# Optimization experiments

Measured on AMD Instinct MI355X. Metric: run time of the kernel, lower is better.

## Reference

```python
import jax, jax.numpy as jnp
import numpy as np

G, N, E, F, H, O, MO = 64, 2048, 16384, 128, 128, 128, 128


def setup_inputs() -> dict:
    key = jax.random.key(0)
    ks = jax.random.split(key, 12)
    # edges: per-graph contiguous blocks, local indices in [0, N-2] (never touch center N-1)
    src_l = jax.random.randint(ks[0], (G, E), 0, N - 1)
    dst_l = jax.random.randint(ks[1], (G, E), 0, N - 1)
    offs = (jnp.arange(G, dtype=jnp.int64) * N)[:, None]
    edge_index = jnp.stack([(src_l + offs).reshape(-1), (dst_l + offs).reshape(-1)]).astype(jnp.int64)
    x = jax.random.normal(ks[2], (G * N, F), dtype=jnp.float32)
    batch = jnp.repeat(jnp.arange(G, dtype=jnp.int64), N)
    center_node_indices = jnp.full((G,), N - 1, dtype=jnp.int64)
    def lin(k, fan_in, shape):
        return jax.random.normal(k, shape, dtype=jnp.float32) / np.sqrt(fan_in)
    return {
        "x": x, "edge_index": edge_index, "batch": batch,
        "center_node_indices": center_node_indices,
        "W1": lin(ks[3], F, (F, H)), "b1": jnp.zeros((H,), jnp.float32),
        "W2": lin(ks[4], F, (F, O)), "b2": jnp.zeros((O,), jnp.float32),
        "W3": lin(ks[5], F, (F, O)), "b3": jnp.zeros((O,), jnp.float32),
        "Wm": lin(ks[6], H + F, (H + F, MO)), "bm": jnp.zeros((MO,), jnp.float32),
    }


def _gcn(x, src, dst, W, b):
    # PyG GCNConv: D^{-1/2}(A+I)D^{-1/2} X W + b, messages src->dst, deg at dst
    n = x.shape[0]
    h = x @ W
    deg = 1.0 + jax.ops.segment_sum(jnp.ones(src.shape[0], h.dtype), dst, num_segments=n)
    dis = jax.lax.rsqrt(deg)
    msg = h[src] * (dis[src] * dis[dst])[:, None]
    agg = jax.ops.segment_sum(msg, dst, num_segments=n)
    return agg + h * (1.0 / deg)[:, None] + b


_gcn_v = jax.vmap(_gcn, in_axes=(0, 0, 0, None, None))


def reference(x, edge_index, batch, center_node_indices, W1, b1, W2, b2, W3, b3, Wm, bm):
    g = center_node_indices.shape[0]
    n = x.shape[0] // g
    e = edge_index.shape[1] // g
    offs = (jnp.arange(g) * n)[:, None]
    src = edge_index[0].reshape(g, e) - offs  # local per-graph edges
    dst = edge_index[1].reshape(g, e) - offs
    xg = x.reshape(g, n, -1)                      # [G,N,F]
    h1 = _gcn_v(xg, src, dst, W1, b1)             # [G,N,H]
    ce = h1[jnp.arange(g), center_node_indices]   # [G,H] center embeddings
    x_nc = xg[:, : n - 1]                         # non-center nodes (center = N-1)
    hd = W1.shape[1]
    # MLP(cat([center_emb, node_feat])) = relu(ce@Wm_top + x@Wm_bot + bm)
    mask = jax.nn.relu((ce @ Wm[:hd])[:, None, :] + x_nc @ Wm[hd:] + bm)  # [G,N-1,MO]
    core = _gcn_v(mask * x_nc, src, dst, W2, b2)          # [G,N-1,O]
    red = _gcn_v((1.0 - mask) * x_nc, src, dst, W3, b3)   # [G,N-1,O]
    return core.mean(axis=0), red.mean(axis=0)
```

## Files before the change

kernel.cpp:

```cpp
#include <hip/hip_runtime.h>

typedef unsigned short u16;
typedef unsigned int uint32;
typedef __bf16 bf16x8 __attribute__((ext_vector_type(8)));
typedef float f32x4 __attribute__((ext_vector_type(4)));

static constexpr int Gg = 64;
static constexpr int Nn = 2048;
static constexpr int Ee = 16384;
static constexpr int GN = Gg * Nn;
static constexpr int GE = Gg * Ee;

__device__ __forceinline__ u16 f2u(float f) {
    uint32 i = __float_as_uint(f);
    uint32 r = (i + 0x7FFFu + ((i >> 16) & 1u)) >> 16;
    return (u16)r;
}
__device__ __forceinline__ float lo16f(uint32 v) { return __uint_as_float(v << 16); }
__device__ __forceinline__ float hi16f(uint32 v) { return __uint_as_float(v & 0xffff0000u); }

__global__ __launch_bounds__(1024) void k_build(const int* __restrict__ ei,
                                                const float* __restrict__ Wm,
                                                const float* __restrict__ x,
                                                const int* __restrict__ center,
                                                const float* __restrict__ W1,
                                                const float* __restrict__ b1,
                                                const float* __restrict__ bm,
                                                float* __restrict__ invdeg,
                                                int* __restrict__ rp, int2* __restrict__ nme,
                                                u16* __restrict__ Wtp,
                                                float* __restrict__ A) {
    int t = threadIdx.x;
    if (blockIdx.x >= 64) {
        int g = blockIdx.x - 64;
        __shared__ float sv[128], sce[128], spart[8][128];
        int seg = t >> 7, ch = t & 127;
        if (t < 128) {
            int cg = (g << 11) + center[g];
            sv[t] = x[cg * 128 + t];
        }
        __syncthreads();
        float p = 0.f;
        #pragma unroll
        for (int f0 = 0; f0 < 16; ++f0) {
            int f = seg * 16 + f0;
            p += sv[f] * W1[f * 128 + ch];
        }
        spart[seg][ch] = p;
        __syncthreads();
        if (t < 128) {
            float a = b1[t];
            #pragma unroll
            for (int s2 = 0; s2 < 8; ++s2) a += spart[s2][t];
            sce[t] = a;
        }
        __syncthreads();
        p = 0.f;
        #pragma unroll
        for (int f0 = 0; f0 < 16; ++f0) {
            int f = seg * 16 + f0;
            p += sce[f] * Wm[f * 128 + ch];
        }
        spart[seg][ch] = p;
        __syncthreads();
        if (t < 128) {
            float a = bm[t];
            #pragma unroll
            for (int s2 = 0; s2 < 8; ++s2) a += spart[s2][t];
            A[g * 128 + t] = a;
        }
        return;
    }

    int g = blockIdx.x;
    __shared__ int h[2048];
    __shared__ float sdis[2048];
    __shared__ int wsum[16];
    int* curs = h;
    h[t] = 0; h[t + 1024] = 0;
    if (t < 256) {
        int tid = g * 256 + t;
        int j = tid & 7, l = (tid >> 3) & 63, kc = tid >> 9;
        int ks = kc >> 3, ct = kc & 7, lm = l & 15, lq = l >> 4;
        int f = ks * 32 + lq * 8 + j, c = ct * 16 + lm;
        Wtp[tid] = f2u(Wm[(128 + f) * 128 + c]);
    }
    __syncthreads();
    #pragma unroll
    for (int k = 0; k < 4; ++k) {
        int4 d4 = *(const int4*)&ei[GE + g * Ee + k * 4096 + t * 4];
        atomicAdd(&h[d4.x & (Nn - 1)], 1);
        atomicAdd(&h[d4.y & (Nn - 1)], 1);
        atomicAdd(&h[d4.z & (Nn - 1)], 1);
        atomicAdd(&h[d4.w & (Nn - 1)], 1);
    }
    __syncthreads();
    int c0 = h[2 * t], c1 = h[2 * t + 1];
    {
        float d0 = 1.0f + (float)c0, d1 = 1.0f + (float)c1;
        sdis[2 * t] = rsqrtf(d0);
        sdis[2 * t + 1] = rsqrtf(d1);
        invdeg[(g << 11) + 2 * t] = 1.0f / d0;
        invdeg[(g << 11) + 2 * t + 1] = 1.0f / d1;
    }
    int val = c0 + c1;
    int lane = t & 63, wv = t >> 6;
    int inc = val;
    #pragma unroll
    for (int off = 1; off < 64; off <<= 1) {
        int n = __shfl_up(inc, off, 64);
        if (lane >= off) inc += n;
    }
    if (lane == 63) wsum[wv] = inc;
    __syncthreads();
    if (wv == 0 && lane < 16) {
        int s2 = wsum[lane];
        #pragma unroll
        for (int off = 1; off < 16; off <<= 1) {
            int n = __shfl_up(s2, off, 16);
            if ((lane & 15) >= off) s2 += n;
        }
        wsum[lane] = s2;
    }
    __syncthreads();
    int excl = inc - val + (wv ? wsum[wv - 1] : 0);
    int base = g * Ee + excl;
    rp[(g << 11) + 2 * t] = base;
    rp[(g << 11) + 2 * t + 1] = base + c0;
    if (g == 63 && t == 1023) rp[GN] = GE;
    curs[2 * t] = base;
    curs[2 * t + 1] = base + c0;
    __syncthreads();
    #pragma unroll
    for (int k = 0; k < 4; ++k) {
        int e = g * Ee + k * 4096 + t * 4;
        int4 s4 = *(const int4*)&ei[e];
        int4 d4 = *(const int4*)&ei[GE + e];
        int p0 = atomicAdd(&curs[d4.x & (Nn - 1)], 1);
        nme[p0] = make_int2(s4.x, __float_as_int(sdis[s4.x & (Nn - 1)] * sdis[d4.x & (Nn - 1)]));
        int p1 = atomicAdd(&curs[d4.y & (Nn - 1)], 1);
        nme[p1] = make_int2(s4.y, __float_as_int(sdis[s4.y & (Nn - 1)] * sdis[d4.y & (Nn - 1)]));
        int p2 = atomicAdd(&curs[d4.z & (Nn - 1)], 1);
        nme[p2] = make_int2(s4.z, __float_as_int(sdis[s4.z & (Nn - 1)] * sdis[d4.z & (Nn - 1)]));
        int p3 = atomicAdd(&curs[d4.w & (Nn - 1)], 1);
        nme[p3] = make_int2(s4.w, __float_as_int(sdis[s4.w & (Nn - 1)] * sdis[d4.w & (Nn - 1)]));
    }
}

__global__ __launch_bounds__(512) void k_masky(const float* __restrict__ x,
                                               const u16* __restrict__ Wtp,
                                               const float* __restrict__ A,
                                               u16* __restrict__ xy) {
    __shared__ u16 sW[16384];
    __shared__ float sA[128];
    int t = threadIdx.x;
    int bp = blockIdx.x;
    int g = bp >> 4;
    {
        const uint4* src = (const uint4*)Wtp;
        uint4* dst = (uint4*)sW;
        #pragma unroll
        for (int k = 0; k < 4; ++k) dst[k * 512 + t] = src[k * 512 + t];
    }
    if (t < 128) sA[t] = A[g * 128 + t];
    __syncthreads();

    int w = t >> 6, l = t & 63;
    int lm = l & 15, lq = l >> 4;
    int row = bp * 128 + w * 16 + lm;
    const float* xrow = x + row * 128;
    const bf16x8* Ap = (const bf16x8*)sW;

    float4 f0 = *(const float4*)(xrow + 0 * 32 + lq * 8);
    float4 f1 = *(const float4*)(xrow + 0 * 32 + lq * 8 + 4);
    float4 f2 = *(const float4*)(xrow + 1 * 32 + lq * 8);
    float4 f3 = *(const float4*)(xrow + 1 * 32 + lq * 8 + 4);
    float4 f4 = *(const float4*)(xrow + 2 * 32 + lq * 8);
    float4 f5 = *(const float4*)(xrow + 2 * 32 + lq * 8 + 4);
    float4 f6 = *(const float4*)(xrow + 3 * 32 + lq * 8);
    float4 f7 = *(const float4*)(xrow + 3 * 32 + lq * 8 + 4);
    union { u16 u[8]; bf16x8 v; } bf[4];
    #define PACK(ks, a, b)                                              \
        bf[ks].u[0] = f2u((a).x); bf[ks].u[1] = f2u((a).y);             \
        bf[ks].u[2] = f2u((a).z); bf[ks].u[3] = f2u((a).w);             \
        bf[ks].u[4] = f2u((b).x); bf[ks].u[5] = f2u((b).y);             \
        bf[ks].u[6] = f2u((b).z); bf[ks].u[7] = f2u((b).w);
    PACK(0, f0, f1) PACK(1, f2, f3) PACK(2, f4, f5) PACK(3, f6, f7)
    #undef PACK

    f32x4 acc[8] = {};
    #pragma unroll
    for (int ks = 0; ks < 4; ++ks) {
        #pragma unroll
        for (int ct = 0; ct < 8; ++ct) {
            bf16x8 a = Ap[(ks * 8 + ct) * 64 + l];
            acc[ct] = __builtin_amdgcn_mfma_f32_16x16x32_bf16(a, bf[ks].v, acc[ct], 0, 0, 0);
        }
    }

    u16* orow = xy + row * 256;
    #pragma unroll
    for (int ct = 0; ct < 8; ++ct) {
        int ch = ct * 16 + lq * 4;
        float4 xv = *(const float4*)(xrow + ch);
        float y0 = fmaxf(acc[ct][0] + sA[ch + 0], 0.f) * xv.x;
        float y1 = fmaxf(acc[ct][1] + sA[ch + 1], 0.f) * xv.y;
        float y2 = fmaxf(acc[ct][2] + sA[ch + 2], 0.f) * xv.z;
        float y3 = fmaxf(acc[ct][3] + sA[ch + 3], 0.f) * xv.w;
        uint4 q;
        q.x = (uint32)f2u(y0)   | ((uint32)f2u(y1)   << 16);
        q.y = (uint32)f2u(xv.x) | ((uint32)f2u(xv.y) << 16);
        q.z = (uint32)f2u(y2)   | ((uint32)f2u(y3)   << 16);
        q.w = (uint32)f2u(xv.z) | ((uint32)f2u(xv.w) << 16);
        *(uint4*)(orow + ct * 32 + lq * 8) = q;
    }
}

#define ACC8(v, cf)                                                     \
    aY0 += (cf) * lo16f((v).x); aY1 += (cf) * hi16f((v).x);             \
    aX0 += (cf) * lo16f((v).y); aX1 += (cf) * hi16f((v).y);             \
    aY2 += (cf) * lo16f((v).z); aY3 += (cf) * hi16f((v).z);             \
    aX2 += (cf) * lo16f((v).w); aX3 += (cf) * hi16f((v).w);

__global__ __launch_bounds__(256) void k_propx(const u16* __restrict__ xy,
                                               const float* __restrict__ invdeg,
                                               const int* __restrict__ rp,
                                               const int2* __restrict__ nme,
                                               float* __restrict__ zp) {
    int b = blockIdx.x;
    int p = b & 3, c = b >> 2;
    int t = threadIdx.x, w = t >> 6, l = t & 63;
    int half = l >> 5, cl = l & 31;
    int i = c * 4 + w;
    float aY0 = 0.f, aY1 = 0.f, aY2 = 0.f, aY3 = 0.f;
    float aX0 = 0.f, aX1 = 0.f, aX2 = 0.f, aX3 = 0.f;

    for (int g8 = 0; g8 < 16; ++g8) {
        int gid = ((p * 16 + g8) << 11) + i;
        if (half == 0) {
            float cf = invdeg[gid];
            uint4 v = *(const uint4*)(xy + (size_t)gid * 256 + cl * 8);
            ACC8(v, cf)
        }
        int j = rp[gid], jend = rp[gid + 1];
        for (; j + 7 < jend; j += 8) {
            int2 m0 = nme[j + half];
            int2 m1 = nme[j + 2 + half];
            int2 m2 = nme[j + 4 + half];
            int2 m3 = nme[j + 6 + half];
            uint4 v0 = *(const uint4*)(xy + (size_t)m0.x * 256 + cl * 8);
            uint4 v1 = *(const uint4*)(xy + (size_t)m1.x * 256 + cl * 8);
            uint4 v2 = *(const uint4*)(xy + (size_t)m2.x * 256 + cl * 8);
            uint4 v3 = *(const uint4*)(xy + (size_t)m3.x * 256 + cl * 8);
            float c0 = __int_as_float(m0.y), c1 = __int_as_float(m1.y);
            float c2 = __int_as_float(m2.y), c3 = __int_as_float(m3.y);
            ACC8(v0, c0) ACC8(v1, c1) ACC8(v2, c2) ACC8(v3, c3)
        }
        for (; j + 3 < jend; j += 4) {
            int2 m0 = nme[j + half];
            int2 m1 = nme[j + 2 + half];
            uint4 v0 = *(const uint4*)(xy + (size_t)m0.x * 256 + cl * 8);
            uint4 v1 = *(const uint4*)(xy + (size_t)m1.x * 256 + cl * 8);
            float c0 = __int_as_float(m0.y), c1 = __int_as_float(m1.y);
            ACC8(v0, c0) ACC8(v1, c1)
        }
        for (; j < jend; j += 2) {
            int idx = j + half;
            if (idx < jend) {
                int2 m = nme[idx];
                uint4 v = *(const uint4*)(xy + (size_t)m.x * 256 + cl * 8);
                float cf = __int_as_float(m.y);
                ACC8(v, cf)
            }
        }
    }

    aY0 += __shfl_xor(aY0, 32, 64); aY1 += __shfl_xor(aY1, 32, 64);
    aX0 += __shfl_xor(aX0, 32, 64); aX1 += __shfl_xor(aX1, 32, 64);
    aY2 += __shfl_xor(aY2, 32, 64); aY3 += __shfl_xor(aY3, 32, 64);
    aX2 += __shfl_xor(aX2, 32, 64); aX3 += __shfl_xor(aX3, 32, 64);
    if (half == 0) {
        float* zr = zp + ((size_t)((p << 11) + i) << 8) + cl * 8;
        *(float4*)(zr) = make_float4(aY0, aY1, aX0, aX1);
        *(float4*)(zr + 4) = make_float4(aY2, aY3, aX2, aX3);
    }
}

__global__ __launch_bounds__(256) void k_reduce(const float* __restrict__ zp,
                                                const float* __restrict__ W2, const float* __restrict__ b2,
                                                const float* __restrict__ W3, const float* __restrict__ b3,
                                                float* __restrict__ out) {
    int i = blockIdx.x;
    int t = threadIdx.x;
    __shared__ float zm[128], zxm[128];
    float s = 0.f;
    #pragma unroll
    for (int p = 0; p < 4; ++p) s += zp[((size_t)((p << 11) + i) << 8) + t];
    s *= (1.0f / 64.0f);
    int k = t >> 2, r = t & 3;
    if (r < 2) zm[2 * k + r] = s; else zxm[2 * k + (r - 2)] = s;
    __syncthreads();
    int cc = t & 127;
    if (t < 128) {
        float acc = b2[cc];
        #pragma unroll 8
        for (int f = 0; f < 128; ++f) acc += zm[f] * W2[f * 128 + cc];
        out[i * 128 + cc] = acc;
    } else {
        float acc = b3[cc];
        #pragma unroll 8
        for (int f = 0; f < 128; ++f) acc += (zxm[f] - zm[f]) * W3[f * 128 + cc];
        out[2047 * 128 + i * 128 + cc] = acc;
    }
}


extern "C" void kernel_launch(void* const* d_in, const int* in_sizes, int n_in,
                              void* d_out, int out_size, void* d_ws, size_t ws_size,
                              hipStream_t stream) {
    const float* x    = (const float*)d_in[0];
    const int* ei     = (const int*)d_in[1];
    const int* center = (const int*)d_in[3];
    const float* W1 = (const float*)d_in[4];
    const float* b1 = (const float*)d_in[5];
    const float* W2 = (const float*)d_in[6];
    const float* b2 = (const float*)d_in[7];
    const float* W3 = (const float*)d_in[8];
    const float* b3 = (const float*)d_in[9];
    const float* Wm = (const float*)d_in[10];
    const float* bm = (const float*)d_in[11];
    float* out = (float*)d_out;

    char* ws = (char*)d_ws;
    float* invdeg = (float*)(ws + 0);
    int*   rp     = (int*)(ws + 524288);
    float* A      = (float*)(ws + 1052672);
    u16*   Wtp    = (u16*)(ws + 1085440);
    int2*  nme    = (int2*)(ws + 1118208);
    float* zp     = (float*)(ws + 9506816);
    u16*   xy     = (u16*)(ws + 26283776);

    k_build<<<dim3(128), dim3(1024), 0, stream>>>(ei, Wm, x, center, W1, b1, bm,
                                                  invdeg, rp, nme, Wtp, A);
    k_masky<<<dim3(1024), dim3(512), 0, stream>>>(x, Wtp, A, xy);
    k_propx<<<dim3(2048), dim3(256), 0, stream>>>(xy, invdeg, rp, nme, zp);
    k_reduce<<<dim3(Nn - 1), dim3(256), 0, stream>>>(zp, W2, b2, W3, b3, out);
}
```

Before: 231.4 us.

## Fuse CSR build and mask MLP kernels into one launch

Merges k_build and k_masky into a single kernel with 1088 blocks: the first 64 build the per-graph CSR, degrees and edge norms, and the rest compute the mask MLP. Each mask block now recomputes the center embedding and its projection, and converts and permutes Wm into bf16 shared memory itself, instead of reading precomputed A and Wtp from global memory. This removes one kernel launch and the serialization between the two stages, letting CSR construction overlap the MFMA work. In exchange every one of the 1024 mask blocks repeats the small matvecs and the 16K-element weight conversion.

```diff
diff --git a/kernel.cpp b/kernel.cpp
--- a/kernel.cpp
+++ b/kernel.cpp
@@ -19,157 +19,134 @@
 __device__ __forceinline__ float lo16f(uint32 v) { return __uint_as_float(v << 16); }
 __device__ __forceinline__ float hi16f(uint32 v) { return __uint_as_float(v & 0xffff0000u); }
 
-__global__ __launch_bounds__(1024) void k_build(const int* __restrict__ ei,
-                                                const float* __restrict__ Wm,
-                                                const float* __restrict__ x,
-                                                const int* __restrict__ center,
-                                                const float* __restrict__ W1,
-                                                const float* __restrict__ b1,
-                                                const float* __restrict__ bm,
-                                                float* __restrict__ invdeg,
-                                                int* __restrict__ rp, int2* __restrict__ nme,
-                                                u16* __restrict__ Wtp,
-                                                float* __restrict__ A) {
+__global__ __launch_bounds__(512) void k_mb(const int* __restrict__ ei,
+                                            const float* __restrict__ Wm,
+                                            const float* __restrict__ x,
+                                            const int* __restrict__ center,
+                                            const float* __restrict__ W1,
+                                            const float* __restrict__ b1,
+                                            const float* __restrict__ bm,
+                                            float* __restrict__ invdeg,
+                                            int* __restrict__ rp, int2* __restrict__ nme,
+                                            u16* __restrict__ xy) {
     int t = threadIdx.x;
-    if (blockIdx.x >= 64) {
-        int g = blockIdx.x - 64;
-        __shared__ float sv[128], sce[128], spart[8][128];
-        int seg = t >> 7, ch = t & 127;
-        if (t < 128) {
-            int cg = (g << 11) + center[g];
-            sv[t] = x[cg * 128 + t];
-        }
-        __syncthreads();
-        float p = 0.f;
+    if (blockIdx.x < 64) {
+        int g = blockIdx.x;
+        __shared__ int h[2048];
+        __shared__ float sdis[2048];
+        __shared__ int wsum[8];
+        int* curs = h;
+        h[t] = 0; h[t + 512] = 0; h[t + 1024] = 0; h[t + 1536] = 0;
+        __syncthreads();
         #pragma unroll
-        for (int f0 = 0; f0 < 16; ++f0) {
-            int f = seg * 16 + f0;
-            p += sv[f] * W1[f * 128 + ch];
-        }
-        spart[seg][ch] = p;
-        __syncthreads();
-        if (t < 128) {
-            float a = b1[t];
+        for (int k = 0; k < 8; ++k) {
+            int4 d4 = *(const int4*)&ei[GE + g * Ee + k * 2048 + t * 4];
+            atomicAdd(&h[d4.x & (Nn - 1)], 1);
+            atomicAdd(&h[d4.y & (Nn - 1)], 1);
+            atomicAdd(&h[d4.z & (Nn - 1)], 1);
+            atomicAdd(&h[d4.w & (Nn - 1)], 1);
+        }
+        __syncthreads();
+        int c0 = h[4 * t], c1 = h[4 * t + 1], c2 = h[4 * t + 2], c3 = h[4 * t + 3];
+        {
+            float d0 = 1.0f + (float)c0, d1 = 1.0f + (float)c1;
+            float d2 = 1.0f + (float)c2, d3 = 1.0f + (float)c3;
+            sdis[4 * t] = rsqrtf(d0);     sdis[4 * t + 1] = rsqrtf(d1);
+            sdis[4 * t + 2] = rsqrtf(d2); sdis[4 * t + 3] = rsqrtf(d3);
+            invdeg[(g << 11) + 4 * t] = 1.0f / d0;
+            invdeg[(g << 11) + 4 * t + 1] = 1.0f / d1;
+            invdeg[(g << 11) + 4 * t + 2] = 1.0f / d2;
+            invdeg[(g << 11) + 4 * t + 3] = 1.0f / d3;
+        }
+        int val = c0 + c1 + c2 + c3;
+        int lane = t & 63, wv = t >> 6;
+        int inc = val;
+        #pragma unroll
+        for (int off = 1; off < 64; off <<= 1) {
+            int n = __shfl_up(inc, off, 64);
+            if (lane >= off) inc += n;
+        }
+        if (lane == 63) wsum[wv] = inc;
+        __syncthreads();
+        if (wv == 0 && lane < 8) {
+            int s2 = wsum[lane];
             #pragma unroll
-            for (int s2 = 0; s2 < 8; ++s2) a += spart[s2][t];
-            sce[t] = a;
-        }
-        __syncthreads();
-        p = 0.f;
+            for (int off = 1; off < 8; off <<= 1) {
+                int n = __shfl_up(s2, off, 8);
+                if (lane >= off) s2 += n;
+            }
+            wsum[lane] = s2;
+        }
+        __syncthreads();
+        int excl = inc - val + (wv ? wsum[wv - 1] : 0);
+        int base = g * Ee + excl;
+        int b1v = base + c0, b2v = b1v + c1, b3v = b2v + c2;
+        rp[(g << 11) + 4 * t] = base;
+        rp[(g << 11) + 4 * t + 1] = b1v;
+        rp[(g << 11) + 4 * t + 2] = b2v;
+        rp[(g << 11) + 4 * t + 3] = b3v;
+        if (g == 63 && t == 511) rp[GN] = GE;
+        curs[4 * t] = base; curs[4 * t + 1] = b1v;
+        curs[4 * t + 2] = b2v; curs[4 * t + 3] = b3v;
+        __syncthreads();
         #pragma unroll
-        for (int f0 = 0; f0 < 16; ++f0) {
-            int f = seg * 16 + f0;
-            p += sce[f] * Wm[f * 128 + ch];
-        }
-        spart[seg][ch] = p;
-        __syncthreads();
-        if (t < 128) {
-            float a = bm[t];
-            #pragma unroll
-            for (int s2 = 0; s2 < 8; ++s2) a += spart[s2][t];
-            A[g * 128 + t] = a;
+        for (int k = 0; k < 8; ++k) {
+            int e = g * Ee + k * 2048 + t * 4;
+            int4 s4 = *(const int4*)&ei[e];
+            int4 d4 = *(const int4*)&ei[GE + e];
+            int p0 = atomicAdd(&curs[d4.x & (Nn - 1)], 1);
+            nme[p0] = make_int2(s4.x, __float_as_int(sdis[s4.x & (Nn - 1)] * sdis[d4.x & (Nn - 1)]));
+            int p1 = atomicAdd(&curs[d4.y & (Nn - 1)], 1);
+            nme[p1] = make_int2(s4.y, __float_as_int(sdis[s4.y & (Nn - 1)] * sdis[d4.y & (Nn - 1)]));
+            int p2 = atomicAdd(&curs[d4.z & (Nn - 1)], 1);
+            nme[p2] = make_int2(s4.z, __float_as_int(sdis[s4.z & (Nn - 1)] * sdis[d4.z & (Nn - 1)]));
+            int p3 = atomicAdd(&curs[d4.w & (Nn - 1)], 1);
+            nme[p3] = make_int2(s4.w, __float_as_int(sdis[s4.w & (Nn - 1)] * sdis[d4.w & (Nn - 1)]));
         }
         return;
     }
 
-    int g = blockIdx.x;
-    __shared__ int h[2048];
-    __shared__ float sdis[2048];
-    __shared__ int wsum[16];
-    int* curs = h;
-    h[t] = 0; h[t + 1024] = 0;
-    if (t < 256) {
-        int tid = g * 256 + t;
-        int j = tid & 7, l = (tid >> 3) & 63, kc = tid >> 9;
-        int ks = kc >> 3, ct = kc & 7, lm = l & 15, lq = l >> 4;
-        int f = ks * 32 + lq * 8 + j, c = ct * 16 + lm;
-        Wtp[tid] = f2u(Wm[(128 + f) * 128 + c]);
-    }
-    __syncthreads();
-    #pragma unroll
-    for (int k = 0; k < 4; ++k) {
-        int4 d4 = *(const int4*)&ei[GE + g * Ee + k * 4096 + t * 4];
-        atomicAdd(&h[d4.x & (Nn - 1)], 1);
-        atomicAdd(&h[d4.y & (Nn - 1)], 1);
-        atomicAdd(&h[d4.z & (Nn - 1)], 1);
-        atomicAdd(&h[d4.w & (Nn - 1)], 1);
-    }
-    __syncthreads();
-    int c0 = h[2 * t], c1 = h[2 * t + 1];
-    {
-        float d0 = 1.0f + (float)c0, d1 = 1.0f + (float)c1;
-        sdis[2 * t] = rsqrtf(d0);
-        sdis[2 * t + 1] = rsqrtf(d1);
-        invdeg[(g << 11) + 2 * t] = 1.0f / d0;
-        invdeg[(g << 11) + 2 * t + 1] = 1.0f / d1;
-    }
-    int val = c0 + c1;
-    int lane = t & 63, wv = t >> 6;
-    int inc = val;
-    #pragma unroll
-    for (int off = 1; off < 64; off <<= 1) {
-        int n = __shfl_up(inc, off, 64);
-        if (lane >= off) inc += n;
-    }
-    if (lane == 63) wsum[wv] = inc;
-    __syncthreads();
-    if (wv == 0 && lane < 16) {
-        int s2 = wsum[lane];
-        #pragma unroll
-        for (int off = 1; off < 16; off <<= 1) {
-            int n = __shfl_up(s2, off, 16);
-            if ((lane & 15) >= off) s2 += n;
-        }
-        wsum[lane] = s2;
-    }
-    __syncthreads();
-    int excl = inc - val + (wv ? wsum[wv - 1] : 0);
-    int base = g * Ee + excl;
-    rp[(g << 11) + 2 * t] = base;
-    rp[(g << 11) + 2 * t + 1] = base + c0;
-    if (g == 63 && t == 1023) rp[GN] = GE;
-    curs[2 * t] = base;
-    curs[2 * t + 1] = base + c0;
-    __syncthreads();
-    #pragma unroll
-    for (int k = 0; k < 4; ++k) {
-        int e = g * Ee + k * 4096 + t * 4;
-        int4 s4 = *(const int4*)&ei[e];
-        int4 d4 = *(const int4*)&ei[GE + e];
-        int p0 = atomicAdd(&curs[d4.x & (Nn - 1)], 1);
-        nme[p0] = make_int2(s4.x, __float_as_int(sdis[s4.x & (Nn - 1)] * sdis[d4.x & (Nn - 1)]));
-        int p1 = atomicAdd(&curs[d4.y & (Nn - 1)], 1);
-        nme[p1] = make_int2(s4.y, __float_as_int(sdis[s4.y & (Nn - 1)] * sdis[d4.y & (Nn - 1)]));
-        int p2 = atomicAdd(&curs[d4.z & (Nn - 1)], 1);
-        nme[p2] = make_int2(s4.z, __float_as_int(sdis[s4.z & (Nn - 1)] * sdis[d4.z & (Nn - 1)]));
-        int p3 = atomicAdd(&curs[d4.w & (Nn - 1)], 1);
-        nme[p3] = make_int2(s4.w, __float_as_int(sdis[s4.w & (Nn - 1)] * sdis[d4.w & (Nn - 1)]));
-    }
-}
-
-__global__ __launch_bounds__(512) void k_masky(const float* __restrict__ x,
-                                               const u16* __restrict__ Wtp,
-                                               const float* __restrict__ A,
-                                               u16* __restrict__ xy) {
+    int bp = blockIdx.x - 64;
+    int g = bp >> 4;
     __shared__ u16 sW[16384];
-    __shared__ float sA[128];
-    int t = threadIdx.x;
-    int bp = blockIdx.x;
-    int g = bp >> 4;
-    {
-        const uint4* src = (const uint4*)Wtp;
-        uint4* dst = (uint4*)sW;
-        #pragma unroll
-        for (int k = 0; k < 4; ++k) dst[k * 512 + t] = src[k * 512 + t];
-    }
-    if (t < 128) sA[t] = A[g * 128 + t];
-    __syncthreads();
+    __shared__ float sA[128], sv[128], sce[128], spart[4][128];
+
+    if (t < 128) sv[t] = x[(size_t)((g << 11) + center[g]) * 128 + t];
+    __syncthreads();
+    int seg = t >> 7, ch = t & 127;
+    float p = 0.f;
+    #pragma unroll
+    for (int f0i = 0; f0i < 32; ++f0i) {
+        int f = seg * 32 + f0i;
+        p += sv[f] * W1[f * 128 + ch];
+    }
+    spart[seg][ch] = p;
+    __syncthreads();
+    if (t < 128) sce[t] = b1[t] + spart[0][t] + spart[1][t] + spart[2][t] + spart[3][t];
+    __syncthreads();
+    p = 0.f;
+    #pragma unroll
+    for (int f0i = 0; f0i < 32; ++f0i) {
+        int f = seg * 32 + f0i;
+        p += sce[f] * Wm[f * 128 + ch];
+    }
+    spart[seg][ch] = p;
+    __syncthreads();
+    if (t < 128) sA[t] = bm[t] + spart[0][t] + spart[1][t] + spart[2][t] + spart[3][t];
+
+    #pragma unroll 4
+    for (int q = 0; q < 32; ++q) {
+        int tid = q * 512 + t;
+        int j = tid & 7, l2 = (tid >> 3) & 63, kc = tid >> 9;
+        int ks = kc >> 3, ct = kc & 7, lm2 = l2 & 15, lq2 = l2 >> 4;
+        int f = ks * 32 + lq2 * 8 + j, c = ct * 16 + lm2;
+        sW[tid] = f2u(Wm[(128 + f) * 128 + c]);
+    }
 
     int w = t >> 6, l = t & 63;
     int lm = l & 15, lq = l >> 4;
     int row = bp * 128 + w * 16 + lm;
-    const float* xrow = x + row * 128;
-    const bf16x8* Ap = (const bf16x8*)sW;
+    const float* xrow = x + (size_t)row * 128;
 
     float4 f0 = *(const float4*)(xrow + 0 * 32 + lq * 8);
     float4 f1 = *(const float4*)(xrow + 0 * 32 + lq * 8 + 4);
@@ -179,6 +156,8 @@
     float4 f5 = *(const float4*)(xrow + 2 * 32 + lq * 8 + 4);
     float4 f6 = *(const float4*)(xrow + 3 * 32 + lq * 8);
     float4 f7 = *(const float4*)(xrow + 3 * 32 + lq * 8 + 4);
+    __syncthreads();
+
     union { u16 u[8]; bf16x8 v; } bf[4];
     #define PACK(ks, a, b)                                              \
         bf[ks].u[0] = f2u((a).x); bf[ks].u[1] = f2u((a).y);             \
@@ -188,6 +167,7 @@
     PACK(0, f0, f1) PACK(1, f2, f3) PACK(2, f4, f5) PACK(3, f6, f7)
     #undef PACK
 
+    const bf16x8* Ap = (const bf16x8*)sW;
     f32x4 acc[8] = {};
     #pragma unroll
     for (int ks = 0; ks < 4; ++ks) {
@@ -198,15 +178,15 @@
         }
     }
 
-    u16* orow = xy + row * 256;
+    u16* orow = xy + (size_t)row * 256;
     #pragma unroll
     for (int ct = 0; ct < 8; ++ct) {
-        int ch = ct * 16 + lq * 4;
-        float4 xv = *(const float4*)(xrow + ch);
-        float y0 = fmaxf(acc[ct][0] + sA[ch + 0], 0.f) * xv.x;
-        float y1 = fmaxf(acc[ct][1] + sA[ch + 1], 0.f) * xv.y;
-        float y2 = fmaxf(acc[ct][2] + sA[ch + 2], 0.f) * xv.z;
-        float y3 = fmaxf(acc[ct][3] + sA[ch + 3], 0.f) * xv.w;
+        int ch2 = ct * 16 + lq * 4;
+        float4 xv = *(const float4*)(xrow + ch2);
+        float y0 = fmaxf(acc[ct][0] + sA[ch2 + 0], 0.f) * xv.x;
+        float y1 = fmaxf(acc[ct][1] + sA[ch2 + 1], 0.f) * xv.y;
+        float y2 = fmaxf(acc[ct][2] + sA[ch2 + 2], 0.f) * xv.z;
+        float y3 = fmaxf(acc[ct][3] + sA[ch2 + 3], 0.f) * xv.w;
         uint4 q;
         q.x = (uint32)f2u(y0)   | ((uint32)f2u(y1)   << 16);
         q.y = (uint32)f2u(xv.x) | ((uint32)f2u(xv.y) << 16);
@@ -334,15 +314,12 @@
     char* ws = (char*)d_ws;
     float* invdeg = (float*)(ws + 0);
     int*   rp     = (int*)(ws + 524288);
-    float* A      = (float*)(ws + 1052672);
-    u16*   Wtp    = (u16*)(ws + 1085440);
-    int2*  nme    = (int2*)(ws + 1118208);
-    float* zp     = (float*)(ws + 9506816);
-    u16*   xy     = (u16*)(ws + 26283776);
-
-    k_build<<<dim3(128), dim3(1024), 0, stream>>>(ei, Wm, x, center, W1, b1, bm,
-                                                  invdeg, rp, nme, Wtp, A);
-    k_masky<<<dim3(1024), dim3(512), 0, stream>>>(x, Wtp, A, xy);
+    int2*  nme    = (int2*)(ws + 1052672);
+    float* zp     = (float*)(ws + 9441280);
+    u16*   xy     = (u16*)(ws + 17829888);
+
+    k_mb<<<dim3(1088), dim3(512), 0, stream>>>(ei, Wm, x, center, W1, b1, bm,
+                                               invdeg, rp, nme, xy);
     k_propx<<<dim3(2048), dim3(256), 0, stream>>>(xy, invdeg, rp, nme, zp);
     k_reduce<<<dim3(Nn - 1), dim3(256), 0, stream>>>(zp, W2, b2, W3, b3, out);
 }
```

Result: faster. 219.3 us (-5.2%).
